# Performance work log

Hardware: AMD Instinct MI355X
Metric: run time of the kernel (lower is better)

Reference implementation:

```python
import jax, jax.numpy as jnp
import numpy as np

B, L, H, D = 16, 2048, 768, 768
M, TPL = 8, 16  # labels per example, tokens per label


def setup_inputs() -> dict:
    key = jax.random.key(0)
    k1, k2, k3, k4 = jax.random.split(key, 4)
    hidden_states = jax.random.normal(k1, (B, L, H), dtype=jnp.float32)
    # first M*TPL tokens are label tokens with ids 1..M, rest are text tokens
    pos = jnp.arange(L)
    row = jnp.where(pos < M * TPL, pos // TPL + 1, 0).astype(jnp.int32)
    lmask = jnp.broadcast_to(row, (B, L))
    input_ids = jax.random.randint(k2, (B, L), 0, 30000, dtype=jnp.int32)
    attention_mask = jnp.ones((B, L), dtype=jnp.int32)
    Wt = jax.random.normal(k3, (H, D), dtype=jnp.float32) / np.sqrt(H)
    bt = jnp.zeros((D,), dtype=jnp.float32)
    Wl = jax.random.normal(k4, (H, D), dtype=jnp.float32) / np.sqrt(H)
    bl = jnp.zeros((D,), dtype=jnp.float32)
    attention_temperature = jnp.array(1.0, dtype=jnp.float32)
    logit_scale = jnp.array(2.0, dtype=jnp.float32)
    return dict(hidden_states=hidden_states, Wt=Wt, bt=bt, Wl=Wl, bl=bl,
                attention_temperature=attention_temperature, logit_scale=logit_scale,
                lmask=lmask, input_ids=input_ids, attention_mask=attention_mask,
                num_labels=M)


def reference(hidden_states, Wt, bt, Wl, bl, attention_temperature, logit_scale,
              lmask, input_ids, attention_mask, num_labels):
    # hidden_states: (B, L, H); lmask: (B, L) int label ids (>0 = label token)
    Bb, Ll, _ = hidden_states.shape
    Mm = num_labels  # static python int (== max label id)
    proj_text = hidden_states @ Wt + bt            # (B, L, D)  text_projector (dropout=eval identity)
    proj_label = hidden_states @ Wl + bl           # (B, L, D)  label_projector on all tokens
    label_tok = lmask > 0                          # (B, L)
    # segment-mean of projected label tokens per (batch, label_id) slot
    flat_idx = jnp.where(label_tok,
                         jnp.arange(Bb, dtype=lmask.dtype)[:, None] * Mm + (lmask - 1),
                         Bb * Mm).reshape(-1)
    masked = proj_label * label_tok[..., None].astype(proj_label.dtype)
    seg = jax.ops.segment_sum(masked.reshape(Bb * Ll, -1), flat_idx,
                              num_segments=Bb * Mm + 1)[: Bb * Mm]
    counts = jax.ops.segment_sum(label_tok.reshape(-1).astype(jnp.float32), flat_idx,
                                 num_segments=Bb * Mm + 1)[: Bb * Mm]
    aggregated_labels = seg / jnp.maximum(counts, 1.0)[:, None]   # (B*M, D)
    agg = aggregated_labels.reshape(Bb, Mm, -1)                   # (B, M, D)
    # attention-weighted text pooling per label over text tokens
    text_mask = (lmask == 0) & (attention_mask == 1)              # (B, L)
    temp = jnp.maximum(jnp.abs(attention_temperature), 0.1)
    scores = jnp.einsum('bmd,bld->bml', agg, proj_text) / temp
    scores = jnp.where(text_mask[:, None, :], scores, -jnp.inf)
    attn = jax.nn.softmax(scores, axis=-1)                        # (B, M, L)
    aggregated_text = jnp.einsum('bml,bld->bmd', attn, proj_text).reshape(Bb * Mm, -1)
    # cosine similarity head with learnable temperature exp(logit_scale)
    tn = aggregated_text / jnp.clip(jnp.linalg.norm(aggregated_text, axis=-1, keepdims=True), 1e-8)
    ln = aggregated_labels / jnp.clip(jnp.linalg.norm(aggregated_labels, axis=-1, keepdims=True), 1e-8)
    scale = jnp.exp(logit_scale)
    logits = jnp.sum(tn * ln, axis=-1, keepdims=True) * scale     # (B*M, 1)
    all_batch_ids = jnp.repeat(jnp.arange(Bb), Mm)
    all_label_ids = jnp.tile(jnp.arange(1, Mm + 1), Bb)
    return (logits, all_batch_ids, all_label_ids, aggregated_labels, scale, aggregated_text)
```

## Files before the change

kernel.cpp:

```cpp
#include <hip/hip_runtime.h>
#include <hip/hip_bf16.h>

typedef __attribute__((ext_vector_type(8))) short s16x8;
typedef __attribute__((ext_vector_type(4))) float f32x4;

#define BB 16
#define LL 2048
#define HH 768
#define DD 768
#define MM 8

#define O_LOGITS 0
#define O_BID    128
#define O_LID    256
#define O_AGGL   384
#define O_SCALE  98688
#define O_AGGT   98689

#define WTT_OFF  0u
#define WLT_OFF  1179648u
#define WTB_OFF  2359296u
#define HBAR_OFF 3538944u
#define QH_OFF   3932160u
#define HST_OFF  4325376u
#define CVEC_OFF 4718592u
#define PML_OFF  4719104u
#define PO_OFF   4751872u
#define SK_OFF   17334784u

__device__ __forceinline__ short f2bf(float x) {
  union { float f; unsigned u; } v; v.f = x;
  unsigned r = v.u + 0x7FFFu + ((v.u >> 16) & 1u);
  return (short)(r >> 16);
}

#define GLOAD_LDS16(gp, lp) __builtin_amdgcn_global_load_lds( \
    (const __attribute__((address_space(1))) unsigned int*)(gp), \
    (__attribute__((address_space(3))) unsigned int*)(lp), 16, 0, 0)

__global__ void k_prep(const float* __restrict__ Wt, const float* __restrict__ Wl,
                       short* __restrict__ Wtt, short* __restrict__ Wlt,
                       short* __restrict__ Wtb,
                       const float* __restrict__ hs, const int* __restrict__ lmask,
                       float* __restrict__ hbar) {
  __shared__ float tile[64][65];
  __shared__ int list[LL];
  __shared__ int nlist_s;
  int bx = blockIdx.x;
  int t = threadIdx.x;
  if (bx < 432) {
    int z = bx / 144, r = bx % 144;
    int kb = (r % 12) * 64, nb = (r / 12) * 64;
    int c = t & 63;
    int r0 = (t >> 6) * 16;
    if (z == 2) {
#pragma unroll
      for (int i = 0; i < 16; ++i) {
        int rr = kb + r0 + i;
        Wtb[(size_t)rr * DD + nb + c] = f2bf(Wt[(size_t)rr * DD + nb + c]);
      }
      return;
    }
    const float* src = z ? Wl : Wt;
    short* dst = z ? Wlt : Wtt;
#pragma unroll
    for (int i = 0; i < 16; ++i)
      tile[r0 + i][c] = src[(size_t)(kb + r0 + i) * DD + nb + c];
    __syncthreads();
#pragma unroll
    for (int i = 0; i < 16; ++i)
      dst[(size_t)(nb + r0 + i) * HH + kb + c] = f2bf(tile[c][r0 + i]);
    return;
  }
  int bh = bx - 432;
  int b = bh >> 3, m = bh & 7;
  int lane = t & 63, w = t >> 6;
  if (w == 0) {
    int base = 0;
    for (int win = 0; win < LL / 64; ++win) {
      int l = win * 64 + lane;
      bool match = (lmask[b * LL + l] == m + 1);
      unsigned long long mk = __ballot(match);
      if (match) {
        int pos = base + (int)__popcll(mk & ((1ull << lane) - 1ull));
        list[pos] = l;
      }
      base += (int)__popcll(mk);
    }
    if (lane == 0) nlist_s = base;
  }
  __syncthreads();
  int n = nlist_s;
  float inv = 1.0f / (float)(n > 1 ? n : 1);
  float a0 = 0.f, a1 = 0.f, a2 = 0.f;
  for (int i = 0; i < n; ++i) {
    const float* rr = hs + (size_t)(b * LL + list[i]) * HH;
    a0 += rr[t]; a1 += rr[t + 256]; a2 += rr[t + 512];
  }
  float* dst = hbar + (size_t)(b * MM + m) * HH;
  dst[t] = a0 * inv; dst[t + 256] = a1 * inv; dst[t + 512] = a2 * inv;
}

__global__ __launch_bounds__(256, 3)
void k_skgemm(const float* __restrict__ A, const short* __restrict__ Bt,
              float* __restrict__ part) {
  __shared__ short As[128][64];
  __shared__ short Bs[2][128][64];
  int t = threadIdx.x;
  int lane = t & 63, w = t >> 6;
  int wm = w >> 1, wn = w & 1;
  int n0 = blockIdx.x * 128;
  int kt0 = blockIdx.y * 3;

  f32x4 acc[4][4] = {};
  float4 areg[8];

  auto issueA = [&](int kt) {
    const float* Ag = A + (size_t)(kt0 + kt) * 64;
#pragma unroll
    for (int i = 0; i < 8; ++i) {
      int slot = i * 256 + t;
      int row = slot >> 4, c = slot & 15;
      areg[i] = *(const float4*)(Ag + (size_t)row * HH + c * 4);
    }
  };
  auto issueB = [&](int kt, int buf) {
    const short* Bg = Bt + (size_t)n0 * HH + (size_t)(kt0 + kt) * 64;
#pragma unroll
    for (int i = 0; i < 4; ++i) {
      int slot = i * 256 + w * 64 + lane;
      int row = slot >> 3, c = slot & 7;
      int cs = c ^ (row & 7);
      GLOAD_LDS16(Bg + (size_t)row * HH + cs * 8,
                  (char*)&Bs[0][0][0] + (size_t)buf * 16384 + (size_t)(i * 256 + w * 64) * 16);
    }
  };
  auto writeA = [&]() {
#pragma unroll
    for (int i = 0; i < 8; ++i) {
      int slot = i * 256 + t;
      int row = slot >> 4, c = slot & 15;
      unsigned d0, d1;
      asm("v_cvt_pk_bf16_f32 %0, %1, %2" : "=v"(d0) : "v"(areg[i].x), "v"(areg[i].y));
      asm("v_cvt_pk_bf16_f32 %0, %1, %2" : "=v"(d1) : "v"(areg[i].z), "v"(areg[i].w));
      int phys = (c >> 1) ^ (row & 7);
      uint2 val = {d0, d1};
      *(uint2*)((char*)&As[0][0] + (size_t)row * 128 + phys * 16 + (c & 1) * 8) = val;
    }
  };
  auto compute = [&](int buf) {
#pragma unroll
    for (int kk = 0; kk < 2; ++kk) {
      s16x8 a[4], bb[4];
#pragma unroll
      for (int i = 0; i < 4; ++i) {
        int row = wm * 64 + i * 16 + (lane & 15);
        int p = (kk * 4 + (lane >> 4)) ^ (row & 7);
        a[i] = *(const s16x8*)((const char*)&As[0][0] + (size_t)row * 128 + p * 16);
      }
#pragma unroll
      for (int i = 0; i < 4; ++i) {
        int row = wn * 64 + i * 16 + (lane & 15);
        int p = (kk * 4 + (lane >> 4)) ^ (row & 7);
        bb[i] = *(const s16x8*)((const char*)&Bs[0][0][0] + (size_t)buf * 16384 + (size_t)row * 128 + p * 16);
      }
#pragma unroll
      for (int mi = 0; mi < 4; ++mi)
#pragma unroll
        for (int ni = 0; ni < 4; ++ni)
          acc[mi][ni] = __builtin_amdgcn_mfma_f32_16x16x32_bf16(a[mi], bb[ni], acc[mi][ni], 0, 0, 0);
    }
  };

  issueA(0); issueB(0, 0);
  writeA();
  __syncthreads();
  for (int kt = 0; kt < 3; ++kt) {
    if (kt + 1 < 3) { issueA(kt + 1); issueB(kt + 1, (kt + 1) & 1); }
    compute(kt & 1);
    __syncthreads();
    if (kt + 1 < 3) {
      writeA();
      __syncthreads();
    }
  }

  float* po = part + (size_t)blockIdx.y * 128 * HH;
#pragma unroll
  for (int mi = 0; mi < 4; ++mi) {
    int row = wm * 64 + mi * 16 + ((lane >> 4) * 4);
#pragma unroll
    for (int ni = 0; ni < 4; ++ni) {
      int col = n0 + wn * 64 + ni * 16 + (lane & 15);
#pragma unroll
      for (int j = 0; j < 4; ++j)
        po[(size_t)(row + j) * HH + col] = acc[mi][ni][j];
    }
  }
}

__global__ void k_red_agg(const float* __restrict__ part, const float* __restrict__ bl,
                          const float* __restrict__ bt, float* __restrict__ out,
                          float* __restrict__ cvec) {
  int row = blockIdx.x;
  int t = threadIdx.x;
  int lane = t & 63, w = t >> 6;
  __shared__ float wred[4];
  float dotbt = 0.f;
#pragma unroll
  for (int cc = 0; cc < 3; ++cc) {
    int c = cc * 256 + t;
    float s = bl[c];
#pragma unroll
    for (int kc = 0; kc < 4; ++kc)
      s += part[((size_t)kc * 128 + row) * HH + c];
    out[O_AGGL + (size_t)row * DD + c] = s;
    dotbt += s * bt[c];
  }
  for (int sh = 32; sh; sh >>= 1) dotbt += __shfl_xor(dotbt, sh, 64);
  if (lane == 0) wred[w] = dotbt;
  __syncthreads();
  if (t == 0) cvec[row] = wred[0] + wred[1] + wred[2] + wred[3];
}

__global__ void k_red_qh(const float* __restrict__ part, float* __restrict__ qh) {
  int row = blockIdx.x;
  int t = threadIdx.x;
#pragma unroll
  for (int cc = 0; cc < 3; ++cc) {
    int c = cc * 256 + t;
    float s = 0.f;
#pragma unroll
    for (int kc = 0; kc < 4; ++kc)
      s += part[((size_t)kc * 128 + row) * HH + c];
    qh[(size_t)row * HH + c] = s;
  }
}

__global__ void k_red_aggt(const float* __restrict__ part, const float* __restrict__ bt,
                           float* __restrict__ out) {
  int row = blockIdx.x;
  int t = threadIdx.x;
#pragma unroll
  for (int cc = 0; cc < 3; ++cc) {
    int c = cc * 256 + t;
    float s = bt[c];
#pragma unroll
    for (int kc = 0; kc < 4; ++kc)
      s += part[((size_t)kc * 128 + row) * HH + c];
    out[O_AGGT + (size_t)row * DD + c] = s;
  }
}

__global__ __launch_bounds__(256, 3)
void k_attnpool(const float* __restrict__ hs, const float* __restrict__ qh,
                const float* __restrict__ cvec, const int* __restrict__ lmask,
                const int* __restrict__ amask, const float* __restrict__ temp_p,
                float* __restrict__ part_o, float* __restrict__ part_ml) {
  __shared__ short As[2][64][64];
  __shared__ short Bs[16][776];
  __shared__ float w_lds[64][8];
  int chunk = blockIdx.x;
  int b = blockIdx.y;
  int t = threadIdx.x;
  int lane = t & 63, w = t >> 6;

  const float* qsrc = qh + (size_t)b * MM * HH;
  for (int c = t; c < HH; c += 256) {
#pragma unroll
    for (int r = 0; r < 8; ++r) Bs[r][c] = f2bf(qsrc[(size_t)r * HH + c]);
#pragma unroll
    for (int r = 8; r < 16; ++r) Bs[r][c] = 0;
  }

  const float* Hg = hs + (size_t)(b * LL + chunk * 64) * HH;
  float4 areg[4];
  auto issueA = [&](int kt) {
#pragma unroll
    for (int i = 0; i < 4; ++i) {
      int slot = i * 256 + t;
      int row = slot >> 4, c = slot & 15;
      areg[i] = *(const float4*)(Hg + (size_t)row * HH + kt * 64 + c * 4);
    }
  };
  auto writeA = [&](int buf) {
#pragma unroll
    for (int i = 0; i < 4; ++i) {
      int slot = i * 256 + t;
      int row = slot >> 4, c = slot & 15;
      unsigned d0, d1;
      asm("v_cvt_pk_bf16_f32 %0, %1, %2" : "=v"(d0) : "v"(areg[i].x), "v"(areg[i].y));
      asm("v_cvt_pk_bf16_f32 %0, %1, %2" : "=v"(d1) : "v"(areg[i].z), "v"(areg[i].w));
      int phys = (c >> 1) ^ (row & 7);
      uint2 val = {d0, d1};
      *(uint2*)((char*)&As[buf][0][0] + (size_t)row * 128 + phys * 16 + (c & 1) * 8) = val;
    }
  };

  f32x4 acc = {};
  issueA(0);
  writeA(0);
  __syncthreads();
  for (int kt = 0; kt < 12; ++kt) {
    if (kt + 1 < 12) issueA(kt + 1);
    int buf = kt & 1;
#pragma unroll
    for (int kk = 0; kk < 2; ++kk) {
      int arow = w * 16 + (lane & 15);
      int p = (kk * 4 + (lane >> 4)) ^ (arow & 7);
      s16x8 a = *(const s16x8*)((const char*)&As[buf][0][0] + (size_t)arow * 128 + p * 16);
      s16x8 bfr = *(const s16x8*)&Bs[lane & 15][kt * 64 + kk * 32 + (lane >> 4) * 8];
      acc = __builtin_amdgcn_mfma_f32_16x16x32_bf16(a, bfr, acc, 0, 0, 0);
    }
    if (kt + 1 < 12) writeA(buf ^ 1);
    __syncthreads();
  }

  float inv_temp = 1.0f / fmaxf(fabsf(temp_p[0]), 0.1f);
  int m = lane & 15;
  int tok0 = w * 16 + (lane >> 4) * 4;
  if (m < MM) {
    float cv = cvec[b * MM + m];
    int4 lm = *(const int4*)&lmask[b * LL + chunk * 64 + tok0];
    int4 am = *(const int4*)&amask[b * LL + chunk * 64 + tok0];
    w_lds[tok0 + 0][m] = (lm.x == 0 && am.x == 1) ? (acc[0] + cv) * inv_temp : -1e30f;
    w_lds[tok0 + 1][m] = (lm.y == 0 && am.y == 1) ? (acc[1] + cv) * inv_temp : -1e30f;
    w_lds[tok0 + 2][m] = (lm.z == 0 && am.z == 1) ? (acc[2] + cv) * inv_temp : -1e30f;
    w_lds[tok0 + 3][m] = (lm.w == 0 && am.w == 1) ? (acc[3] + cv) * inv_temp : -1e30f;
  }
  __syncthreads();

#pragma unroll
  for (int half = 0; half < 2; ++half) {
    int mm = w + half * 4;
    float v = w_lds[lane][mm];
    float mx = v;
    for (int s = 32; s; s >>= 1) mx = fmaxf(mx, __shfl_xor(mx, s, 64));
    float e = __expf(v - mx);
    float l = e;
    for (int s = 32; s; s >>= 1) l += __shfl_xor(l, s, 64);
    w_lds[lane][mm] = e;
    if (lane == 0) {
      float* pml = part_ml + ((size_t)(chunk * BB + b) * MM + mm) * 2;
      pml[0] = mx; pml[1] = l;
    }
  }
  __syncthreads();

  if (t < 192) {
    int h0 = t * 4;
    f32x4 o[8] = {};
    const float* hp = Hg + h0;
    for (int tok = 0; tok < 64; ++tok) {
      float4 hv = *(const float4*)(hp + (size_t)tok * HH);
      float4 w0 = *(const float4*)&w_lds[tok][0];
      float4 w1 = *(const float4*)&w_lds[tok][4];
      o[0][0] += w0.x * hv.x; o[0][1] += w0.x * hv.y; o[0][2] += w0.x * hv.z; o[0][3] += w0.x * hv.w;
      o[1][0] += w0.y * hv.x; o[1][1] += w0.y * hv.y; o[1][2] += w0.y * hv.z; o[1][3] += w0.y * hv.w;
      o[2][0] += w0.z * hv.x; o[2][1] += w0.z * hv.y; o[2][2] += w0.z * hv.z; o[2][3] += w0.z * hv.w;
      o[3][0] += w0.w * hv.x; o[3][1] += w0.w * hv.y; o[3][2] += w0.w * hv.z; o[3][3] += w0.w * hv.w;
      o[4][0] += w1.x * hv.x; o[4][1] += w1.x * hv.y; o[4][2] += w1.x * hv.z; o[4][3] += w1.x * hv.w;
      o[5][0] += w1.y * hv.x; o[5][1] += w1.y * hv.y; o[5][2] += w1.y * hv.z; o[5][3] += w1.y * hv.w;
      o[6][0] += w1.z * hv.x; o[6][1] += w1.z * hv.y; o[6][2] += w1.z * hv.z; o[6][3] += w1.z * hv.w;
      o[7][0] += w1.w * hv.x; o[7][1] += w1.w * hv.y; o[7][2] += w1.w * hv.z; o[7][3] += w1.w * hv.w;
    }
    float* po = part_o + (size_t)(chunk * BB + b) * MM * HH + h0;
#pragma unroll
    for (int mm = 0; mm < 8; ++mm)
      *(f32x4*)(po + (size_t)mm * HH) = o[mm];
  }
}

__global__ void k_finish(const float* __restrict__ part_o, const float* __restrict__ part_ml,
                         float* __restrict__ hst) {
  int row = blockIdx.x;
  int b = row >> 3, m = row & 7;
  int t = threadIdx.x;
  float mg = -1e30f;
#pragma unroll
  for (int lc = 0; lc < 32; ++lc)
    mg = fmaxf(mg, part_ml[((size_t)(lc * BB + b) * MM + m) * 2]);
  float L = 0.f;
  f32x4 acc = {};
  int h0 = t * 4;
  for (int lc = 0; lc < 32; ++lc) {
    const float* pml = part_ml + ((size_t)(lc * BB + b) * MM + m) * 2;
    float f = __expf(pml[0] - mg);
    L += pml[1] * f;
    f32x4 v = *(const f32x4*)(part_o + ((size_t)(lc * BB + b) * MM + m) * HH + h0);
    acc[0] += v[0] * f; acc[1] += v[1] * f; acc[2] += v[2] * f; acc[3] += v[3] * f;
  }
  float inv = 1.0f / L;
  f32x4 r = {acc[0] * inv, acc[1] * inv, acc[2] * inv, acc[3] * inv};
  *(f32x4*)(hst + (size_t)row * HH + h0) = r;
}

__global__ void k_head(const float* __restrict__ lscale_p, float* __restrict__ out) {
  int row = blockIdx.x;
  int lane = threadIdx.x;
  const float* at = out + O_AGGT + (size_t)row * DD;
  const float* al = out + O_AGGL + (size_t)row * DD;
  float dot = 0.f, nt = 0.f, nl = 0.f;
  for (int i = lane; i < DD; i += 64) {
    float a = at[i], c = al[i];
    dot += a * c; nt += a * a; nl += c * c;
  }
  for (int s = 32; s; s >>= 1) {
    dot += __shfl_xor(dot, s, 64);
    nt  += __shfl_xor(nt, s, 64);
    nl  += __shfl_xor(nl, s, 64);
  }
  if (lane == 0) {
    float scale = expf(lscale_p[0]);
    float denom = fmaxf(sqrtf(nt), 1e-8f) * fmaxf(sqrtf(nl), 1e-8f);
    out[O_LOGITS + row] = dot / denom * scale;
    out[O_BID + row] = (float)(row >> 3);
    out[O_LID + row] = (float)((row & 7) + 1);
    if (row == 0) out[O_SCALE] = scale;
  }
}

extern "C" void kernel_launch(void* const* d_in, const int* in_sizes, int n_in,
                              void* d_out, int out_size, void* d_ws, size_t ws_size,
                              hipStream_t stream) {
  const float* hs    = (const float*)d_in[0];
  const float* Wt    = (const float*)d_in[1];
  const float* bt    = (const float*)d_in[2];
  const float* Wl    = (const float*)d_in[3];
  const float* bl    = (const float*)d_in[4];
  const float* atemp = (const float*)d_in[5];
  const float* lsc   = (const float*)d_in[6];
  const int*   lmask = (const int*)d_in[7];
  const int*   amask = (const int*)d_in[9];
  float* out = (float*)d_out;
  char* ws = (char*)d_ws;
  short* Wtt  = (short*)(ws + WTT_OFF);
  short* Wlt  = (short*)(ws + WLT_OFF);
  short* Wtb  = (short*)(ws + WTB_OFF);
  float* hbar = (float*)(ws + HBAR_OFF);
  float* qh   = (float*)(ws + QH_OFF);
  float* hst  = (float*)(ws + HST_OFF);
  float* cvec = (float*)(ws + CVEC_OFF);
  float* pml  = (float*)(ws + PML_OFF);
  float* po   = (float*)(ws + PO_OFF);
  float* skp  = (float*)(ws + SK_OFF);

  k_prep<<<560, 256, 0, stream>>>(Wt, Wl, Wtt, Wlt, Wtb, hs, lmask, hbar);
  k_skgemm<<<dim3(6, 4), 256, 0, stream>>>(hbar, Wlt, skp);
  k_red_agg<<<128, 256, 0, stream>>>(skp, bl, bt, out, cvec);
  k_skgemm<<<dim3(6, 4), 256, 0, stream>>>(out + O_AGGL, Wtb, skp);
  k_red_qh<<<128, 256, 0, stream>>>(skp, qh);
  k_attnpool<<<dim3(32, 16), 256, 0, stream>>>(hs, qh, cvec, lmask, amask, atemp, po, pml);
  k_finish<<<128, 192, 0, stream>>>(po, pml, hst);
  k_skgemm<<<dim3(6, 4), 256, 0, stream>>>(hst, Wtt, skp);
  k_red_aggt<<<128, 256, 0, stream>>>(skp, bt, out);
  k_head<<<128, 64, 0, stream>>>(lsc, out);
}
```

Baseline: 87.92 us.

## Load GEMM operands directly from global memory and fuse aggt reduction into head

The split-K GEMM and the attention-pooling kernel no longer stage operands through shared memory. They load fp32/bf16 fragments straight from global memory into registers, convert them to bf16 inline, and drop all block barriers. The separate aggregated-text reduction kernel is folded into the head kernel, which removes one launch. The intent is to cut LDS staging, barrier and launch overhead on these small GEMMs. In exchange, global loads become uncoalesced and redundant, and the query rows in attnpool are reloaded and reconverted on every iteration.

```diff
diff --git a/kernel.cpp b/kernel.cpp
--- a/kernel.cpp
+++ b/kernel.cpp
@@ -34,9 +34,14 @@
   return (short)(r >> 16);
 }
 
-#define GLOAD_LDS16(gp, lp) __builtin_amdgcn_global_load_lds( \
-    (const __attribute__((address_space(1))) unsigned int*)(gp), \
-    (__attribute__((address_space(3))) unsigned int*)(lp), 16, 0, 0)
+__device__ __forceinline__ s16x8 cvt8(float4 x0, float4 x1) {
+  union { unsigned u[4]; s16x8 v; } r;
+  asm("v_cvt_pk_bf16_f32 %0, %1, %2" : "=v"(r.u[0]) : "v"(x0.x), "v"(x0.y));
+  asm("v_cvt_pk_bf16_f32 %0, %1, %2" : "=v"(r.u[1]) : "v"(x0.z), "v"(x0.w));
+  asm("v_cvt_pk_bf16_f32 %0, %1, %2" : "=v"(r.u[2]) : "v"(x1.x), "v"(x1.y));
+  asm("v_cvt_pk_bf16_f32 %0, %1, %2" : "=v"(r.u[3]) : "v"(x1.z), "v"(x1.w));
+  return r.v;
+}
 
 __global__ void k_prep(const float* __restrict__ Wt, const float* __restrict__ Wl,
                        short* __restrict__ Wtt, short* __restrict__ Wlt,
@@ -101,87 +106,36 @@
   dst[t] = a0 * inv; dst[t + 256] = a1 * inv; dst[t + 512] = a2 * inv;
 }
 
-__global__ __launch_bounds__(256, 3)
+__global__ __launch_bounds__(256)
 void k_skgemm(const float* __restrict__ A, const short* __restrict__ Bt,
               float* __restrict__ part) {
-  __shared__ short As[128][64];
-  __shared__ short Bs[2][128][64];
   int t = threadIdx.x;
   int lane = t & 63, w = t >> 6;
   int wm = w >> 1, wn = w & 1;
   int n0 = blockIdx.x * 128;
   int kt0 = blockIdx.y * 3;
+  int colofs = (lane >> 4) * 8;
 
   f32x4 acc[4][4] = {};
-  float4 areg[8];
-
-  auto issueA = [&](int kt) {
-    const float* Ag = A + (size_t)(kt0 + kt) * 64;
-#pragma unroll
-    for (int i = 0; i < 8; ++i) {
-      int slot = i * 256 + t;
-      int row = slot >> 4, c = slot & 15;
-      areg[i] = *(const float4*)(Ag + (size_t)row * HH + c * 4);
-    }
-  };
-  auto issueB = [&](int kt, int buf) {
-    const short* Bg = Bt + (size_t)n0 * HH + (size_t)(kt0 + kt) * 64;
-#pragma unroll
-    for (int i = 0; i < 4; ++i) {
-      int slot = i * 256 + w * 64 + lane;
-      int row = slot >> 3, c = slot & 7;
-      int cs = c ^ (row & 7);
-      GLOAD_LDS16(Bg + (size_t)row * HH + cs * 8,
-                  (char*)&Bs[0][0][0] + (size_t)buf * 16384 + (size_t)(i * 256 + w * 64) * 16);
-    }
-  };
-  auto writeA = [&]() {
-#pragma unroll
-    for (int i = 0; i < 8; ++i) {
-      int slot = i * 256 + t;
-      int row = slot >> 4, c = slot & 15;
-      unsigned d0, d1;
-      asm("v_cvt_pk_bf16_f32 %0, %1, %2" : "=v"(d0) : "v"(areg[i].x), "v"(areg[i].y));
-      asm("v_cvt_pk_bf16_f32 %0, %1, %2" : "=v"(d1) : "v"(areg[i].z), "v"(areg[i].w));
-      int phys = (c >> 1) ^ (row & 7);
-      uint2 val = {d0, d1};
-      *(uint2*)((char*)&As[0][0] + (size_t)row * 128 + phys * 16 + (c & 1) * 8) = val;
-    }
-  };
-  auto compute = [&](int buf) {
+#pragma unroll
+  for (int kt = 0; kt < 3; ++kt) {
 #pragma unroll
     for (int kk = 0; kk < 2; ++kk) {
+      int c = (kt0 + kt) * 64 + kk * 32 + colofs;
       s16x8 a[4], bb[4];
 #pragma unroll
       for (int i = 0; i < 4; ++i) {
-        int row = wm * 64 + i * 16 + (lane & 15);
-        int p = (kk * 4 + (lane >> 4)) ^ (row & 7);
-        a[i] = *(const s16x8*)((const char*)&As[0][0] + (size_t)row * 128 + p * 16);
+        const float* ap = A + (size_t)(wm * 64 + i * 16 + (lane & 15)) * HH + c;
+        a[i] = cvt8(*(const float4*)ap, *(const float4*)(ap + 4));
       }
 #pragma unroll
-      for (int i = 0; i < 4; ++i) {
-        int row = wn * 64 + i * 16 + (lane & 15);
-        int p = (kk * 4 + (lane >> 4)) ^ (row & 7);
-        bb[i] = *(const s16x8*)((const char*)&Bs[0][0][0] + (size_t)buf * 16384 + (size_t)row * 128 + p * 16);
-      }
+      for (int i = 0; i < 4; ++i)
+        bb[i] = *(const s16x8*)(Bt + (size_t)(n0 + wn * 64 + i * 16 + (lane & 15)) * HH + c);
 #pragma unroll
       for (int mi = 0; mi < 4; ++mi)
 #pragma unroll
         for (int ni = 0; ni < 4; ++ni)
           acc[mi][ni] = __builtin_amdgcn_mfma_f32_16x16x32_bf16(a[mi], bb[ni], acc[mi][ni], 0, 0, 0);
-    }
-  };
-
-  issueA(0); issueB(0, 0);
-  writeA();
-  __syncthreads();
-  for (int kt = 0; kt < 3; ++kt) {
-    if (kt + 1 < 3) { issueA(kt + 1); issueB(kt + 1, (kt + 1) & 1); }
-    compute(kt & 1);
-    __syncthreads();
-    if (kt + 1 < 3) {
-      writeA();
-      __syncthreads();
     }
   }
 
@@ -237,83 +191,34 @@
   }
 }
 
-__global__ void k_red_aggt(const float* __restrict__ part, const float* __restrict__ bt,
-                           float* __restrict__ out) {
-  int row = blockIdx.x;
-  int t = threadIdx.x;
-#pragma unroll
-  for (int cc = 0; cc < 3; ++cc) {
-    int c = cc * 256 + t;
-    float s = bt[c];
-#pragma unroll
-    for (int kc = 0; kc < 4; ++kc)
-      s += part[((size_t)kc * 128 + row) * HH + c];
-    out[O_AGGT + (size_t)row * DD + c] = s;
-  }
-}
-
-__global__ __launch_bounds__(256, 3)
+__global__ __launch_bounds__(256)
 void k_attnpool(const float* __restrict__ hs, const float* __restrict__ qh,
                 const float* __restrict__ cvec, const int* __restrict__ lmask,
                 const int* __restrict__ amask, const float* __restrict__ temp_p,
                 float* __restrict__ part_o, float* __restrict__ part_ml) {
-  __shared__ short As[2][64][64];
-  __shared__ short Bs[16][776];
   __shared__ float w_lds[64][8];
   int chunk = blockIdx.x;
   int b = blockIdx.y;
   int t = threadIdx.x;
   int lane = t & 63, w = t >> 6;
-
-  const float* qsrc = qh + (size_t)b * MM * HH;
-  for (int c = t; c < HH; c += 256) {
-#pragma unroll
-    for (int r = 0; r < 8; ++r) Bs[r][c] = f2bf(qsrc[(size_t)r * HH + c]);
-#pragma unroll
-    for (int r = 8; r < 16; ++r) Bs[r][c] = 0;
-  }
+  int colofs = (lane >> 4) * 8;
 
   const float* Hg = hs + (size_t)(b * LL + chunk * 64) * HH;
-  float4 areg[4];
-  auto issueA = [&](int kt) {
-#pragma unroll
-    for (int i = 0; i < 4; ++i) {
-      int slot = i * 256 + t;
-      int row = slot >> 4, c = slot & 15;
-      areg[i] = *(const float4*)(Hg + (size_t)row * HH + kt * 64 + c * 4);
-    }
-  };
-  auto writeA = [&](int buf) {
-#pragma unroll
-    for (int i = 0; i < 4; ++i) {
-      int slot = i * 256 + t;
-      int row = slot >> 4, c = slot & 15;
-      unsigned d0, d1;
-      asm("v_cvt_pk_bf16_f32 %0, %1, %2" : "=v"(d0) : "v"(areg[i].x), "v"(areg[i].y));
-      asm("v_cvt_pk_bf16_f32 %0, %1, %2" : "=v"(d1) : "v"(areg[i].z), "v"(areg[i].w));
-      int phys = (c >> 1) ^ (row & 7);
-      uint2 val = {d0, d1};
-      *(uint2*)((char*)&As[buf][0][0] + (size_t)row * 128 + phys * 16 + (c & 1) * 8) = val;
-    }
-  };
+  const float* Arow = Hg + (size_t)(w * 16 + (lane & 15)) * HH;
+  bool bvalid = (lane & 15) < MM;
+  const float* Brow = qh + (size_t)(b * MM + ((lane & 15) & 7)) * HH;
 
   f32x4 acc = {};
-  issueA(0);
-  writeA(0);
-  __syncthreads();
+#pragma unroll
   for (int kt = 0; kt < 12; ++kt) {
-    if (kt + 1 < 12) issueA(kt + 1);
-    int buf = kt & 1;
 #pragma unroll
     for (int kk = 0; kk < 2; ++kk) {
-      int arow = w * 16 + (lane & 15);
-      int p = (kk * 4 + (lane >> 4)) ^ (arow & 7);
-      s16x8 a = *(const s16x8*)((const char*)&As[buf][0][0] + (size_t)arow * 128 + p * 16);
-      s16x8 bfr = *(const s16x8*)&Bs[lane & 15][kt * 64 + kk * 32 + (lane >> 4) * 8];
+      int c = kt * 64 + kk * 32 + colofs;
+      s16x8 a = cvt8(*(const float4*)(Arow + c), *(const float4*)(Arow + c + 4));
+      s16x8 bfr = cvt8(*(const float4*)(Brow + c), *(const float4*)(Brow + c + 4));
+      if (!bvalid) bfr = (s16x8){0, 0, 0, 0, 0, 0, 0, 0};
       acc = __builtin_amdgcn_mfma_f32_16x16x32_bf16(a, bfr, acc, 0, 0, 0);
     }
-    if (kt + 1 < 12) writeA(buf ^ 1);
-    __syncthreads();
   }
 
   float inv_temp = 1.0f / fmaxf(fabsf(temp_p[0]), 0.1f);
@@ -395,14 +300,19 @@
   *(f32x4*)(hst + (size_t)row * HH + h0) = r;
 }
 
-__global__ void k_head(const float* __restrict__ lscale_p, float* __restrict__ out) {
+__global__ void k_head(const float* __restrict__ part, const float* __restrict__ bt,
+                       const float* __restrict__ lscale_p, float* __restrict__ out) {
   int row = blockIdx.x;
   int lane = threadIdx.x;
-  const float* at = out + O_AGGT + (size_t)row * DD;
   const float* al = out + O_AGGL + (size_t)row * DD;
   float dot = 0.f, nt = 0.f, nl = 0.f;
   for (int i = lane; i < DD; i += 64) {
-    float a = at[i], c = al[i];
+    float a = bt[i];
+#pragma unroll
+    for (int kc = 0; kc < 4; ++kc)
+      a += part[((size_t)kc * 128 + row) * HH + i];
+    out[O_AGGT + (size_t)row * DD + i] = a;
+    float c = al[i];
     dot += a * c; nt += a * a; nl += c * c;
   }
   for (int s = 32; s; s >>= 1) {
@@ -453,6 +363,5 @@
   k_attnpool<<<dim3(32, 16), 256, 0, stream>>>(hs, qh, cvec, lmask, amask, atemp, po, pml);
   k_finish<<<128, 192, 0, stream>>>(po, pml, hst);
   k_skgemm<<<dim3(6, 4), 256, 0, stream>>>(hst, Wtt, skp);
-  k_red_aggt<<<128, 256, 0, stream>>>(skp, bt, out);
-  k_head<<<128, 64, 0, stream>>>(lsc, out);
-}
+  k_head<<<128, 64, 0, stream>>>(skp, bt, lsc, out);
+}
```

After: 111.7 us. +27.1%, slower.
